# Performance work log

Hardware: AMD Instinct MI355X
Metric: run time of the kernel (lower is better)

The kernel has to match this reference:

```python
import jax, jax.numpy as jnp
import numpy as np

EPS = 1e-5
NEG_SLOPE = 0.01  # torch LeakyReLU default


def setup_inputs() -> dict:
    key = jax.random.key(0)
    k1, k2 = jax.random.split(key)
    B, C, N, OUT = 4, 256, 4096, 256
    stdv = 1.0 / np.sqrt(OUT)
    x = jax.random.normal(k1, (B, C, N), dtype=jnp.float32)
    W = jax.random.uniform(k2, (C, OUT), dtype=jnp.float32, minval=-stdv, maxval=stdv)
    gamma = jnp.ones((OUT,), dtype=jnp.float32)
    beta = jnp.zeros((OUT,), dtype=jnp.float32)
    return {"x": x, "W": W, "gamma": gamma, "beta": beta}


def reference(x, W, gamma, beta):
    # x: [B, C, N] -> xt: [B, N, C]
    xt = jnp.transpose(x, (0, 2, 1))
    # adjacency: softmax over last dim of [B, N, N] self-similarity (L2=False path)
    scores = jnp.einsum('bnc,bmc->bnm', xt, xt)
    adj = jax.nn.softmax(scores, axis=-1)
    # support: [B, N, OUT]
    support = jnp.einsum('bnc,co->bno', xt, W)
    # output: [B, OUT, N]
    out = jnp.transpose(jnp.einsum('bnm,bmo->bno', adj, support), (0, 2, 1))
    y = jnp.where(out >= 0, out, NEG_SLOPE * out)  # LeakyReLU
    # BatchNorm1d (training mode): per-channel stats over batch and spatial dims
    mean = jnp.mean(y, axis=(0, 2), keepdims=True)
    var = jnp.mean(jnp.square(y - mean), axis=(0, 2), keepdims=True)
    y_hat = (y - mean) * jax.lax.rsqrt(var + EPS)
    return gamma[None, :, None] * y_hat + beta[None, :, None]
```

## Files before the change

### kernel.cpp

```cpp
#include <hip/hip_runtime.h>

typedef _Float16 f16;
typedef _Float16 f16x2 __attribute__((ext_vector_type(2)));
typedef _Float16 f16x4 __attribute__((ext_vector_type(4)));
typedef _Float16 f16x8 __attribute__((ext_vector_type(8)));
typedef float f32x4 __attribute__((ext_vector_type(4)));
typedef float f32x16 __attribute__((ext_vector_type(16)));
typedef int i32x2 __attribute__((ext_vector_type(2)));

#define B_   4
#define C_   256
#define N_   4096
#define OUT_ 256

__device__ __forceinline__ void gld_lds16(const f16* g, f16* l) {
    __builtin_amdgcn_global_load_lds(
        (const __attribute__((address_space(1))) void*)g,
        (__attribute__((address_space(3))) void*)l, 16, 0, 0);
}

__device__ __forceinline__ i32x2 perm32(float x) {
    return __builtin_amdgcn_permlane32_swap(__float_as_int(x), __float_as_int(x), false, false);
}

__global__ __launch_bounds__(256) void k_prep(const float* __restrict__ x,
                                              const float* __restrict__ W,
                                              f16* __restrict__ xt,
                                              f16* __restrict__ Wt,
                                              float* __restrict__ stats) {
    int bid = blockIdx.x;
    int t = threadIdx.x;
    if (bid < 1024) {
        int b  = bid >> 8;
        int ct = (bid >> 6) & 3;
        int nt = bid & 63;
        int c0 = ct * 64, n0 = nt * 64;
        __shared__ float tile[64][65];
        int nl = t & 63;
        int r0 = t >> 6;
        #pragma unroll
        for (int i = 0; i < 16; ++i) {
            int cl = i * 4 + r0;
            tile[cl][nl] = x[((b * C_ + c0 + cl) * N_) + n0 + nl];
        }
        __syncthreads();
        #pragma unroll
        for (int i = 0; i < 4; ++i) {
            int n  = i * 16 + (t >> 4);
            int c4 = (t & 15) * 4;
            f16x4 o = { (f16)tile[c4][n], (f16)tile[c4 + 1][n],
                        (f16)tile[c4 + 2][n], (f16)tile[c4 + 3][n] };
            *(f16x4*)&xt[((b * N_ + n0 + n) * C_) + c0 + c4] = o;
        }
    } else {
        int wb = bid - 1024;
        #pragma unroll
        for (int i = 0; i < 4; ++i) {
            int idx = wb * 1024 + i * 256 + t;
            int c = idx >> 8, o = idx & 255;
            Wt[o * C_ + c] = (f16)W[idx];
        }
        if (wb < 2) stats[wb * 256 + t] = 0.f;
    }
}

__global__ __launch_bounds__(256) void k_support(const f16* __restrict__ xt,
                                                 const f16* __restrict__ Wt,
                                                 f16* __restrict__ supT) {
    int bid0 = blockIdx.x;
    int bid = (bid0 & 7) * 128 + (bid0 >> 3);
    int b  = bid >> 8;
    int ot = (bid >> 6) & 3;
    int mt = bid & 63;
    int o0 = ot * 64, m0 = mt * 64;
    __shared__ __align__(16) f16 Ws[64][264];
    __shared__ __align__(16) f16 Xs[64][264];
    int t = threadIdx.x;
    int wave = t >> 6, lane = t & 63, q = lane >> 4, l15 = lane & 15;
    #pragma unroll
    for (int p = 0; p < 8; ++p) {
        int idx = p * 256 + t;
        int row = idx >> 5, ch = (idx & 31) * 8;
        *(uint4*)&Ws[row][ch] = *(const uint4*)&Wt[(o0 + row) * C_ + ch];
        *(uint4*)&Xs[row][ch] = *(const uint4*)&xt[((b * N_) + m0 + row) * C_ + ch];
    }
    __syncthreads();
    f32x4 acc[4] = {};
    #pragma unroll
    for (int kk = 0; kk < 8; ++kk) {
        f16x8 a = *(f16x8*)&Ws[16 * wave + l15][kk * 32 + q * 8];
        #pragma unroll
        for (int ct = 0; ct < 4; ++ct) {
            f16x8 bb = *(f16x8*)&Xs[16 * ct + l15][kk * 32 + q * 8];
            acc[ct] = __builtin_amdgcn_mfma_f32_16x16x32_f16(a, bb, acc[ct], 0, 0, 0);
        }
    }
    #pragma unroll
    for (int ct = 0; ct < 4; ++ct)
        #pragma unroll
        for (int r = 0; r < 4; ++r) {
            int og = o0 + 16 * wave + q * 4 + r;
            int mg = m0 + 16 * ct + l15;
            supT[((b * OUT_ + og) * N_) + mg] = (f16)acc[ct][r];
        }
}

__global__ __launch_bounds__(256) __attribute__((amdgpu_waves_per_eu(2, 2)))
void k_flash(const f16* __restrict__ xt,
             const f16* __restrict__ supT,
             f16* __restrict__ Op,
             float* __restrict__ Ml) {
    int bid0 = blockIdx.x;
    int wg = (bid0 & 7) * 64 + (bid0 >> 3);
    int h  = wg >> 8;
    int b  = (wg >> 6) & 3;
    int n0 = (wg & 63) * 64;

    __shared__ __align__(16) f16 KsL[2][64 * 256];
    __shared__ __align__(16) f16 Ps[64][72];
    __shared__ float Lh[2][64];
    __shared__ float Lt[64];

    int t = threadIdx.x;
    int wave = t >> 6, lane = t & 63;
    int q = lane >> 4, l15 = lane & 15;
    int l31 = lane & 31, hi = lane >> 5;
    int nh = wave & 1, mh = wave >> 1;

    const f16* qbase = xt + ((size_t)(b * N_) + n0 + 32 * nh + l31) * C_ + 8 * hi;
    f16x8 qf[16];
    #pragma unroll
    for (int kc = 0; kc < 16; ++kc)
        qf[kc] = *(const f16x8*)&qbase[16 * kc];

    float m_fix;
    {
        float s = 0.f;
        #pragma unroll
        for (int kc = 0; kc < 16; ++kc)
            #pragma unroll
            for (int j = 0; j < 8; ++j) {
                float v = (float)qf[kc][j];
                s += v * v;
            }
        i32x2 rr = perm32(s);
        m_fix = __int_as_float(rr[0]) + __int_as_float(rr[1]);
    }

    f32x4 oacc[4][4] = {};
    float l_run = 0.f;

    const f16* kbase = xt + (size_t)b * N_ * C_;
    int c16 = (lane & 31) * 8;
    int rhalf = lane >> 5;
    int soff[8];
    #pragma unroll
    for (int j = 0; j < 8; ++j) {
        int row = wave * 16 + j * 2 + rhalf;
        soff[j] = row * 256 + (c16 ^ ((row & 7) << 3));
    }
    int swr = (l31 & 7) << 3;

    const f16* vbbase = supT + ((size_t)(b * OUT_) + 64 * wave + l15) * N_ + q * 8;

    {
        const f16* kt = kbase + (size_t)(h * 2048) * C_;
        #pragma unroll
        for (int j = 0; j < 8; ++j)
            gld_lds16(kt + soff[j], &KsL[0][wave * 4096 + j * 512]);
    }

    int cur = 0;
    for (int it = 0; it < 32; ++it) {
        int m0 = h * 2048 + it * 64;
        __syncthreads();

        f16x8 vf[2][4];
        const f16* vb = vbbase + m0;
        #pragma unroll
        for (int ks = 0; ks < 2; ++ks)
            #pragma unroll
            for (int ot = 0; ot < 4; ++ot)
                vf[ks][ot] = *(const f16x8*)&vb[(size_t)(16 * ot) * N_ + ks * 32];

        if (it < 31) {
            const f16* kt = kbase + (size_t)(m0 + 64) * C_;
            #pragma unroll
            for (int j = 0; j < 8; ++j)
                gld_lds16(kt + soff[j], &KsL[cur ^ 1][wave * 4096 + j * 512]);
        }

        f32x16 sacc = {};
        const f16* krow = &KsL[cur][(32 * mh + l31) * 256];
        __builtin_amdgcn_s_setprio(1);
        #pragma unroll
        for (int kc = 0; kc < 16; ++kc) {
            int col = (16 * kc + 8 * hi) ^ swr;
            f16x8 kf = *(const f16x8*)&krow[col];
            sacc = __builtin_amdgcn_mfma_f32_32x32x16_f16(kf, qf[kc], sacc, 0, 0, 0);
        }
        __builtin_amdgcn_s_setprio(0);

        float p[16];
        #pragma unroll
        for (int r = 0; r < 16; ++r)
            p[r] = __expf(sacc[r] - m_fix);
        float s0 = (p[0] + p[1]) + (p[2] + p[3]);
        float s1 = (p[4] + p[5]) + (p[6] + p[7]);
        float s2 = (p[8] + p[9]) + (p[10] + p[11]);
        float s3 = (p[12] + p[13]) + (p[14] + p[15]);
        l_run += (s0 + s1) + (s2 + s3);

        #pragma unroll
        for (int g = 0; g < 4; ++g) {
            f16x4 pk = { (f16)p[4 * g], (f16)p[4 * g + 1],
                         (f16)p[4 * g + 2], (f16)p[4 * g + 3] };
            *(f16x4*)&Ps[32 * nh + l31][32 * mh + 8 * g + 4 * hi] = pk;
        }

        asm volatile("s_waitcnt lgkmcnt(0)" ::: "memory");
        __builtin_amdgcn_s_barrier();
        __builtin_amdgcn_sched_barrier(0);

        __builtin_amdgcn_s_setprio(1);
        #pragma unroll
        for (int ks = 0; ks < 2; ++ks) {
            f16x8 af[4];
            #pragma unroll
            for (int nt = 0; nt < 4; ++nt)
                af[nt] = *(f16x8*)&Ps[16 * nt + l15][ks * 32 + q * 8];
            #pragma unroll
            for (int nt = 0; nt < 4; ++nt)
                #pragma unroll
                for (int ot = 0; ot < 4; ++ot)
                    oacc[nt][ot] = __builtin_amdgcn_mfma_f32_16x16x32_f16(af[nt], vf[ks][ot], oacc[nt][ot], 0, 0, 0);
        }
        __builtin_amdgcn_s_setprio(0);
        cur ^= 1;
    }

    {
        i32x2 rr = perm32(l_run);
        l_run = __int_as_float(rr[0]) + __int_as_float(rr[1]);
    }
    __syncthreads();
    if (lane < 32) Lh[mh][32 * nh + l31] = l_run;
    __syncthreads();
    if (t < 64) {
        float lt = Lh[0][t] + Lh[1][t];
        Lt[t] = 1.0f / fmaxf(lt, 1e-37f);
        Ml[(size_t)wg * 64 + t] = lt;
    }
    __syncthreads();

    float4 lv[4];
    #pragma unroll
    for (int nt = 0; nt < 4; ++nt)
        lv[nt] = *(const float4*)&Lt[16 * nt + 4 * q];

    f16* Obase = Op + (size_t)wg * (64 * 256);
    #pragma unroll
    for (int nt = 0; nt < 4; ++nt)
        #pragma unroll
        for (int ot = 0; ot < 4; ++ot)
            #pragma unroll
            for (int r = 0; r < 4; ++r) {
                int n = 16 * nt + q * 4 + r;
                int o = 64 * wave + 16 * ot + l15;
                Obase[n * 256 + o] = (f16)(oacc[nt][ot][r] * ((const float*)&lv[nt])[r]);
            }
}

__global__ __launch_bounds__(256) void k_mstats(const f16* __restrict__ Op,
                                                const float* __restrict__ Ml,
                                                float* __restrict__ stats) {
    int bid0 = blockIdx.x;
    int bid = (bid0 & 7) * 128 + (bid0 >> 3);
    int b  = bid >> 8;
    int nb = (bid >> 2) & 63;
    int oq = bid & 3;
    int o0 = oq * 64;
    int t = threadIdx.x;
    const f16* O1 = Op + (size_t)(b * 64 + nb) * (64 * 256);
    const f16* O2 = Op + (size_t)(b * 64 + nb + 256) * (64 * 256);
    const float* Ml1 = Ml + (size_t)(b * 64 + nb) * 64;
    const float* Ml2 = Ml + (size_t)(b * 64 + nb + 256) * 64;
    __shared__ float c1s[64], c2s[64];
    __shared__ float rs[8][64], rss[8][64];
    if (t < 64) {
        float l1 = Ml1[t], l2 = Ml2[t];
        float inv = 1.0f / (l1 + l2);
        c1s[t] = l1 * inv;
        c2s[t] = l2 * inv;
    }
    __syncthreads();
    int ow = (t & 31) * 2;
    int ng = t >> 5;
    float s0 = 0.f, s1 = 0.f, ss0 = 0.f, ss1 = 0.f;
    #pragma unroll
    for (int j = 0; j < 8; ++j) {
        int n = ng * 8 + j;
        f16x2 u1 = *(const f16x2*)&O1[n * 256 + o0 + ow];
        f16x2 u2 = *(const f16x2*)&O2[n * 256 + o0 + ow];
        float c1 = c1s[n], c2 = c2s[n];
        float v0 = c1 * (float)u1[0] + c2 * (float)u2[0];
        float v1 = c1 * (float)u1[1] + c2 * (float)u2[1];
        v0 = v0 >= 0.f ? v0 : 0.01f * v0;
        v1 = v1 >= 0.f ? v1 : 0.01f * v1;
        s0 += v0; ss0 += v0 * v0;
        s1 += v1; ss1 += v1 * v1;
    }
    rs[ng][ow] = s0;  rs[ng][ow + 1] = s1;
    rss[ng][ow] = ss0; rss[ng][ow + 1] = ss1;
    __syncthreads();
    if (t < 64) {
        float S = 0.f, SS = 0.f;
        #pragma unroll
        for (int g = 0; g < 8; ++g) { S += rs[g][t]; SS += rss[g][t]; }
        atomicAdd(&stats[o0 + t], S);
        atomicAdd(&stats[256 + o0 + t], SS);
    }
}

__global__ __launch_bounds__(256) void k_mapply(const f16* __restrict__ Op,
                                                const float* __restrict__ Ml,
                                                const float* __restrict__ stats,
                                                const float* __restrict__ gamma,
                                                const float* __restrict__ beta,
                                                float* __restrict__ out) {
    int bid0 = blockIdx.x;
    int bid = (bid0 & 7) * 128 + (bid0 >> 3);
    int b  = bid >> 8;
    int nb = (bid >> 2) & 63;
    int oq = bid & 3;
    int n0 = nb * 64, o0 = oq * 64;
    int t = threadIdx.x;
    const f16* O1 = Op + (size_t)(b * 64 + nb) * (64 * 256);
    const f16* O2 = Op + (size_t)(b * 64 + nb + 256) * (64 * 256);
    const float* Ml1 = Ml + (size_t)(b * 64 + nb) * 64;
    const float* Ml2 = Ml + (size_t)(b * 64 + nb + 256) * 64;
    __shared__ float c1s[64], c2s[64], gs[64], bs[64];
    __shared__ float tile[64][65];
    if (t < 64) {
        float l1 = Ml1[t], l2 = Ml2[t];
        float inv = 1.0f / (l1 + l2);
        c1s[t] = l1 * inv;
        c2s[t] = l2 * inv;
        int o = o0 + t;
        float mean = stats[o] * (1.0f / 16384.0f);
        float var = stats[256 + o] * (1.0f / 16384.0f) - mean * mean;
        float rstd = rsqrtf(var + 1e-5f);
        float g = gamma[o] * rstd;
        gs[t] = g;
        bs[t] = beta[o] - mean * g;
    }
    __syncthreads();
    int ow = (t & 31) * 2;
    int ng = t >> 5;
    #pragma unroll
    for (int j = 0; j < 8; ++j) {
        int n = ng * 8 + j;
        f16x2 u1 = *(const f16x2*)&O1[n * 256 + o0 + ow];
        f16x2 u2 = *(const f16x2*)&O2[n * 256 + o0 + ow];
        float c1 = c1s[n], c2 = c2s[n];
        float v0 = c1 * (float)u1[0] + c2 * (float)u2[0];
        float v1 = c1 * (float)u1[1] + c2 * (float)u2[1];
        v0 = v0 >= 0.f ? v0 : 0.01f * v0;
        v1 = v1 >= 0.f ? v1 : 0.01f * v1;
        tile[ow][n]     = gs[ow] * v0 + bs[ow];
        tile[ow + 1][n] = gs[ow + 1] * v1 + bs[ow + 1];
    }
    __syncthreads();
    int w = t >> 6, lane = t & 63;
    float* dst = out + ((size_t)(b * OUT_ + o0)) * N_ + n0;
    #pragma unroll
    for (int k = 0; k < 16; ++k) {
        int o = 16 * w + k;
        dst[(size_t)o * N_ + lane] = tile[o][lane];
    }
}

extern "C" void kernel_launch(void* const* d_in, const int* in_sizes, int n_in,
                              void* d_out, int out_size, void* d_ws, size_t ws_size,
                              hipStream_t stream) {
    const float* x     = (const float*)d_in[0];
    const float* W     = (const float*)d_in[1];
    const float* gamma = (const float*)d_in[2];
    const float* beta  = (const float*)d_in[3];
    float* out = (float*)d_out;

    f16* xt    = (f16*)d_ws;
    f16* supT  = xt + (size_t)B_ * N_ * C_;
    f16* Wt    = supT + (size_t)B_ * N_ * OUT_;
    f16* Op    = Wt + C_ * OUT_;
    float* Ml  = (float*)(Op + (size_t)2 * 256 * 64 * 256);
    float* stats = Ml + (size_t)512 * 128;

    k_prep<<<1088, 256, 0, stream>>>(x, W, xt, Wt, stats);
    k_support<<<1024, 256, 0, stream>>>(xt, Wt, supT);
    k_flash<<<512, 256, 0, stream>>>(xt, supT, Op, Ml);
    k_mstats<<<1024, 256, 0, stream>>>(Op, Ml, stats);
    k_mapply<<<1024, 256, 0, stream>>>(Op, Ml, stats, gamma, beta, out);
}
```

Baseline: 179.8 us.

## Keep softmax probabilities in registers via permlane swaps and split PV by key half

The flash kernel no longer stages P through shared memory. Lane swaps rearrange the 32x32 score accumulator into the A-operand layout of 32x32x16 MFMAs. Each wave now multiplies its own key half against all 256 output channels, which removes the per-iteration P write/read and one barrier. In exchange, each block now writes four partial outputs instead of two, so partial-output stores and the loads in the stats and apply kernels double. V tiles are also loaded from global inside the loop without prefetch, and the loop-top barrier now waits on all outstanding memory operations.

```diff
diff --git a/kernel.cpp b/kernel.cpp
--- a/kernel.cpp
+++ b/kernel.cpp
@@ -7,6 +7,7 @@
 typedef float f32x4 __attribute__((ext_vector_type(4)));
 typedef float f32x16 __attribute__((ext_vector_type(16)));
 typedef int i32x2 __attribute__((ext_vector_type(2)));
+typedef int i32x4 __attribute__((ext_vector_type(4)));
 
 #define B_   4
 #define C_   256
@@ -19,8 +20,15 @@
         (__attribute__((address_space(3))) void*)l, 16, 0, 0);
 }
 
-__device__ __forceinline__ i32x2 perm32(float x) {
+__device__ __forceinline__ i32x2 perm32(int x) {
+    return __builtin_amdgcn_permlane32_swap(x, x, false, false);
+}
+__device__ __forceinline__ i32x2 perm32f(float x) {
     return __builtin_amdgcn_permlane32_swap(__float_as_int(x), __float_as_int(x), false, false);
+}
+__device__ __forceinline__ int packh(float a, float b) {
+    f16x2 w = { (f16)a, (f16)b };
+    return *(int*)&w;
 }
 
 __global__ __launch_bounds__(256) void k_prep(const float* __restrict__ x,
@@ -114,16 +122,15 @@
     int wg = (bid0 & 7) * 64 + (bid0 >> 3);
     int h  = wg >> 8;
     int b  = (wg >> 6) & 3;
-    int n0 = (wg & 63) * 64;
+    int nb = wg & 63;
+    int n0 = nb * 64;
 
     __shared__ __align__(16) f16 KsL[2][64 * 256];
-    __shared__ __align__(16) f16 Ps[64][72];
     __shared__ float Lh[2][64];
     __shared__ float Lt[64];
 
     int t = threadIdx.x;
     int wave = t >> 6, lane = t & 63;
-    int q = lane >> 4, l15 = lane & 15;
     int l31 = lane & 31, hi = lane >> 5;
     int nh = wave & 1, mh = wave >> 1;
 
@@ -143,11 +150,11 @@
                 float v = (float)qf[kc][j];
                 s += v * v;
             }
-        i32x2 rr = perm32(s);
+        i32x2 rr = perm32f(s);
         m_fix = __int_as_float(rr[0]) + __int_as_float(rr[1]);
     }
 
-    f32x4 oacc[4][4] = {};
+    f32x16 oacc[8] = {};
     float l_run = 0.f;
 
     const f16* kbase = xt + (size_t)b * N_ * C_;
@@ -161,7 +168,7 @@
     }
     int swr = (l31 & 7) << 3;
 
-    const f16* vbbase = supT + ((size_t)(b * OUT_) + 64 * wave + l15) * N_ + q * 8;
+    const f16* vbase = supT + ((size_t)(b * OUT_) + l31) * N_ + 32 * mh + 8 * hi;
 
     {
         const f16* kt = kbase + (size_t)(h * 2048) * C_;
@@ -170,28 +177,22 @@
             gld_lds16(kt + soff[j], &KsL[0][wave * 4096 + j * 512]);
     }
 
-    int cur = 0;
     for (int it = 0; it < 32; ++it) {
         int m0 = h * 2048 + it * 64;
-        __syncthreads();
-
-        f16x8 vf[2][4];
-        const f16* vb = vbbase + m0;
-        #pragma unroll
-        for (int ks = 0; ks < 2; ++ks)
-            #pragma unroll
-            for (int ot = 0; ot < 4; ++ot)
-                vf[ks][ot] = *(const f16x8*)&vb[(size_t)(16 * ot) * N_ + ks * 32];
+
+        asm volatile("s_waitcnt vmcnt(0) lgkmcnt(0)" ::: "memory");
+        __builtin_amdgcn_s_barrier();
+        __builtin_amdgcn_sched_barrier(0);
 
         if (it < 31) {
             const f16* kt = kbase + (size_t)(m0 + 64) * C_;
             #pragma unroll
             for (int j = 0; j < 8; ++j)
-                gld_lds16(kt + soff[j], &KsL[cur ^ 1][wave * 4096 + j * 512]);
+                gld_lds16(kt + soff[j], &KsL[(it + 1) & 1][wave * 4096 + j * 512]);
         }
 
         f32x16 sacc = {};
-        const f16* krow = &KsL[cur][(32 * mh + l31) * 256];
+        const f16* krow = &KsL[it & 1][(32 * mh + l31) * 256];
         __builtin_amdgcn_s_setprio(1);
         #pragma unroll
         for (int kc = 0; kc < 16; ++kc) {
@@ -211,36 +212,34 @@
         float s3 = (p[12] + p[13]) + (p[14] + p[15]);
         l_run += (s0 + s1) + (s2 + s3);
 
-        #pragma unroll
-        for (int g = 0; g < 4; ++g) {
-            f16x4 pk = { (f16)p[4 * g], (f16)p[4 * g + 1],
-                         (f16)p[4 * g + 2], (f16)p[4 * g + 3] };
-            *(f16x4*)&Ps[32 * nh + l31][32 * mh + 8 * g + 4 * hi] = pk;
-        }
-
-        asm volatile("s_waitcnt lgkmcnt(0)" ::: "memory");
-        __builtin_amdgcn_s_barrier();
-        __builtin_amdgcn_sched_barrier(0);
-
+        int U0 = packh(p[0], p[1]),   U1 = packh(p[2], p[3]);
+        int U2 = packh(p[4], p[5]),   U3 = packh(p[6], p[7]);
+        int U4 = packh(p[8], p[9]),   U5 = packh(p[10], p[11]);
+        int U6 = packh(p[12], p[13]), U7 = packh(p[14], p[15]);
+        i32x2 P0 = perm32(U0), P1 = perm32(U1), P2 = perm32(U2), P3 = perm32(U3);
+        i32x2 P4 = perm32(U4), P5 = perm32(U5), P6 = perm32(U6), P7 = perm32(U7);
+        bool hb = hi != 0;
+        i32x4 pa0i = { hb ? P2[0] : P0[0], hb ? P3[0] : P1[0],
+                       hb ? P2[1] : P0[1], hb ? P3[1] : P1[1] };
+        i32x4 pa1i = { hb ? P6[0] : P4[0], hb ? P7[0] : P5[0],
+                       hb ? P6[1] : P4[1], hb ? P7[1] : P5[1] };
+        f16x8 pa0 = *(f16x8*)&pa0i;
+        f16x8 pa1 = *(f16x8*)&pa1i;
+
+        const f16* vb = vbase + m0;
         __builtin_amdgcn_s_setprio(1);
         #pragma unroll
-        for (int ks = 0; ks < 2; ++ks) {
-            f16x8 af[4];
-            #pragma unroll
-            for (int nt = 0; nt < 4; ++nt)
-                af[nt] = *(f16x8*)&Ps[16 * nt + l15][ks * 32 + q * 8];
-            #pragma unroll
-            for (int nt = 0; nt < 4; ++nt)
-                #pragma unroll
-                for (int ot = 0; ot < 4; ++ot)
-                    oacc[nt][ot] = __builtin_amdgcn_mfma_f32_16x16x32_f16(af[nt], vf[ks][ot], oacc[nt][ot], 0, 0, 0);
+        for (int ot = 0; ot < 8; ++ot) {
+            f16x8 v0 = *(const f16x8*)&vb[(size_t)(32 * ot) * N_];
+            f16x8 v1 = *(const f16x8*)&vb[(size_t)(32 * ot) * N_ + 16];
+            oacc[ot] = __builtin_amdgcn_mfma_f32_32x32x16_f16(pa0, v0, oacc[ot], 0, 0, 0);
+            oacc[ot] = __builtin_amdgcn_mfma_f32_32x32x16_f16(pa1, v1, oacc[ot], 0, 0, 0);
         }
         __builtin_amdgcn_s_setprio(0);
-        cur ^= 1;
     }
 
     {
-        i32x2 rr = perm32(l_run);
+        i32x2 rr = perm32f(l_run);
         l_run = __int_as_float(rr[0]) + __int_as_float(rr[1]);
     }
     __syncthreads();
@@ -253,22 +252,20 @@
     }
     __syncthreads();
 
-    float4 lv[4];
-    #pragma unroll
-    for (int nt = 0; nt < 4; ++nt)
-        lv[nt] = *(const float4*)&Lt[16 * nt + 4 * q];
-
-    f16* Obase = Op + (size_t)wg * (64 * 256);
-    #pragma unroll
-    for (int nt = 0; nt < 4; ++nt)
-        #pragma unroll
-        for (int ot = 0; ot < 4; ++ot)
+    f16* Obase = Op + (size_t)((h * 2 + mh) * 256 + b * 64 + nb) * (64 * 256);
+    #pragma unroll
+    for (int g = 0; g < 4; ++g) {
+        float4 lt4 = *(const float4*)&Lt[32 * nh + 8 * g + 4 * hi];
+        #pragma unroll
+        for (int r = 0; r < 4; ++r) {
+            int n_loc = 32 * nh + 8 * g + 4 * hi + r;
+            float sc = ((const float*)&lt4)[r];
             #pragma unroll
-            for (int r = 0; r < 4; ++r) {
-                int n = 16 * nt + q * 4 + r;
-                int o = 64 * wave + 16 * ot + l15;
-                Obase[n * 256 + o] = (f16)(oacc[nt][ot][r] * ((const float*)&lv[nt])[r]);
-            }
+            for (int ot = 0; ot < 8; ++ot)
+                Obase[n_loc * 256 + 32 * ot + l31] =
+                    (f16)(oacc[ot][4 * g + r] * sc);
+        }
+    }
 }
 
 __global__ __launch_bounds__(256) void k_mstats(const f16* __restrict__ Op,
@@ -281,10 +278,12 @@
     int oq = bid & 3;
     int o0 = oq * 64;
     int t = threadIdx.x;
-    const f16* O1 = Op + (size_t)(b * 64 + nb) * (64 * 256);
-    const f16* O2 = Op + (size_t)(b * 64 + nb + 256) * (64 * 256);
+    const f16* Pc[4];
+    #pragma unroll
+    for (int pc = 0; pc < 4; ++pc)
+        Pc[pc] = Op + (size_t)(pc * 256 + b * 64 + nb) * (64 * 256);
     const float* Ml1 = Ml + (size_t)(b * 64 + nb) * 64;
-    const float* Ml2 = Ml + (size_t)(b * 64 + nb + 256) * 64;
+    const float* Ml2 = Ml + (size_t)(256 + b * 64 + nb) * 64;
     __shared__ float c1s[64], c2s[64];
     __shared__ float rs[8][64], rss[8][64];
     if (t < 64) {
@@ -300,11 +299,13 @@
     #pragma unroll
     for (int j = 0; j < 8; ++j) {
         int n = ng * 8 + j;
-        f16x2 u1 = *(const f16x2*)&O1[n * 256 + o0 + ow];
-        f16x2 u2 = *(const f16x2*)&O2[n * 256 + o0 + ow];
+        f16x2 u0 = *(const f16x2*)&Pc[0][n * 256 + o0 + ow];
+        f16x2 u1 = *(const f16x2*)&Pc[1][n * 256 + o0 + ow];
+        f16x2 u2 = *(const f16x2*)&Pc[2][n * 256 + o0 + ow];
+        f16x2 u3 = *(const f16x2*)&Pc[3][n * 256 + o0 + ow];
         float c1 = c1s[n], c2 = c2s[n];
-        float v0 = c1 * (float)u1[0] + c2 * (float)u2[0];
-        float v1 = c1 * (float)u1[1] + c2 * (float)u2[1];
+        float v0 = c1 * ((float)u0[0] + (float)u1[0]) + c2 * ((float)u2[0] + (float)u3[0]);
+        float v1 = c1 * ((float)u0[1] + (float)u1[1]) + c2 * ((float)u2[1] + (float)u3[1]);
         v0 = v0 >= 0.f ? v0 : 0.01f * v0;
         v1 = v1 >= 0.f ? v1 : 0.01f * v1;
         s0 += v0; ss0 += v0 * v0;
@@ -335,10 +336,12 @@
     int oq = bid & 3;
     int n0 = nb * 64, o0 = oq * 64;
     int t = threadIdx.x;
-    const f16* O1 = Op + (size_t)(b * 64 + nb) * (64 * 256);
-    const f16* O2 = Op + (size_t)(b * 64 + nb + 256) * (64 * 256);
+    const f16* Pc[4];
+    #pragma unroll
+    for (int pc = 0; pc < 4; ++pc)
+        Pc[pc] = Op + (size_t)(pc * 256 + b * 64 + nb) * (64 * 256);
     const float* Ml1 = Ml + (size_t)(b * 64 + nb) * 64;
-    const float* Ml2 = Ml + (size_t)(b * 64 + nb + 256) * 64;
+    const float* Ml2 = Ml + (size_t)(256 + b * 64 + nb) * 64;
     __shared__ float c1s[64], c2s[64], gs[64], bs[64];
     __shared__ float tile[64][65];
     if (t < 64) {
@@ -360,11 +363,13 @@
     #pragma unroll
     for (int j = 0; j < 8; ++j) {
         int n = ng * 8 + j;
-        f16x2 u1 = *(const f16x2*)&O1[n * 256 + o0 + ow];
-        f16x2 u2 = *(const f16x2*)&O2[n * 256 + o0 + ow];
+        f16x2 u0 = *(const f16x2*)&Pc[0][n * 256 + o0 + ow];
+        f16x2 u1 = *(const f16x2*)&Pc[1][n * 256 + o0 + ow];
+        f16x2 u2 = *(const f16x2*)&Pc[2][n * 256 + o0 + ow];
+        f16x2 u3 = *(const f16x2*)&Pc[3][n * 256 + o0 + ow];
         float c1 = c1s[n], c2 = c2s[n];
-        float v0 = c1 * (float)u1[0] + c2 * (float)u2[0];
-        float v1 = c1 * (float)u1[1] + c2 * (float)u2[1];
+        float v0 = c1 * ((float)u0[0] + (float)u1[0]) + c2 * ((float)u2[0] + (float)u3[0]);
+        float v1 = c1 * ((float)u0[1] + (float)u1[1]) + c2 * ((float)u2[1] + (float)u3[1]);
         v0 = v0 >= 0.f ? v0 : 0.01f * v0;
         v1 = v1 >= 0.f ? v1 : 0.01f * v1;
         tile[ow][n]     = gs[ow] * v0 + bs[ow];
@@ -393,8 +398,8 @@
     f16* supT  = xt + (size_t)B_ * N_ * C_;
     f16* Wt    = supT + (size_t)B_ * N_ * OUT_;
     f16* Op    = Wt + C_ * OUT_;
-    float* Ml  = (float*)(Op + (size_t)2 * 256 * 64 * 256);
-    float* stats = Ml + (size_t)512 * 128;
+    float* Ml  = (float*)(Op + (size_t)4 * 256 * 64 * 256);
+    float* stats = Ml + (size_t)512 * 64;
 
     k_prep<<<1088, 256, 0, stream>>>(x, W, xt, Wt, stats);
     k_support<<<1024, 256, 0, stream>>>(xt, Wt, supT);
```

Measured after the change: 260.9 us. +45.1%, slower.
